# Kernel optimization log

Measured on AMD Instinct MI355X. Metric: run time of the kernel, lower is better.

Reference implementation:

```python
import jax, jax.numpy as jnp
import numpy as np

L = 12    # AttentionalGNN layers: ['self','cross'] * 6
NH = 4    # heads (hardcoded in AttentionalGNN)
D = 256   # d_model / feature_dim
B, N, M = 2, 2048, 2048
EPS = 1e-5


def conv1x1(W, b, x):
    # Conv1d(kernel_size=1): W [O, I], b [O], x [B, I, N] -> [B, O, N]
    return jnp.einsum('oi,bin->bon', W, x) + b[None, :, None]


def mha(x, src, Wq, bq, Wk, bk, Wv, bv, Wm, bm):
    b_, d_, n_ = x.shape
    dh = d_ // NH
    split = lambda t: t.reshape(b_, dh, NH, t.shape[-1])  # view(b, dim, heads, -1)
    q = split(conv1x1(Wq, bq, x))
    k = split(conv1x1(Wk, bk, src))
    v = split(conv1x1(Wv, bv, src))
    scores = jnp.einsum('bdhn,bdhm->bhnm', q, k) / dh ** 0.5
    prob = jax.nn.softmax(scores, axis=-1)
    msg = jnp.einsum('bhnm,bdhm->bdhn', prob, v).reshape(b_, d_, n_)
    return conv1x1(Wm, bm, msg)


def prop_layer(x, src, Wq, bq, Wk, bk, Wv, bv, Wm, bm, W1, b1, g, bt, W2, b2):
    msg = mha(x, src, Wq, bq, Wk, bk, Wv, bv, Wm, bm)
    h = conv1x1(W1, b1, jnp.concatenate([x, msg], axis=1))
    # BatchNorm1d in inference mode (running_mean=0, running_var=1)
    h = g[None, :, None] * (h * np.float32(1.0 / np.sqrt(1.0 + EPS))) + bt[None, :, None]
    h = jax.nn.relu(h)
    return conv1x1(W2, b2, h)


def setup_inputs() -> dict:
    key = jax.random.key(0)
    ks = jax.random.split(key, 16)
    s = 0.05
    rn = lambda k, sh: jax.random.normal(k, sh, jnp.float32) * s
    return {
        'desc0': jax.random.normal(ks[0], (B, D, N), jnp.float32),
        'desc1': jax.random.normal(ks[1], (B, D, M), jnp.float32),
        'Wq': rn(ks[2], (L, D, D)), 'bq': rn(ks[3], (L, D)),
        'Wk': rn(ks[4], (L, D, D)), 'bk': rn(ks[5], (L, D)),
        'Wv': rn(ks[6], (L, D, D)), 'bv': rn(ks[7], (L, D)),
        'Wm': rn(ks[8], (L, D, D)), 'bm': rn(ks[9], (L, D)),
        'W1': rn(ks[10], (L, 2 * D, 2 * D)), 'b1': rn(ks[11], (L, 2 * D)),
        'gamma': jnp.ones((L, 2 * D), jnp.float32),
        'beta': jnp.zeros((L, 2 * D), jnp.float32),
        'W2': rn(ks[12], (L, D, 2 * D)),
        'b2': jnp.zeros((L, D), jnp.float32),  # nn.init.constant_(mlp[-1].bias, 0)
    }


def reference(desc0, desc1, Wq, bq, Wk, bk, Wv, bv, Wm, bm, W1, b1, gamma, beta, W2, b2):
    for i in range(L):
        cross = (i % 2 == 1)
        src0, src1 = (desc1, desc0) if cross else (desc0, desc1)
        p = (Wq[i], bq[i], Wk[i], bk[i], Wv[i], bv[i], Wm[i], bm[i],
             W1[i], b1[i], gamma[i], beta[i], W2[i], b2[i])
        d0 = prop_layer(desc0, src0, *p)
        d1 = prop_layer(desc1, src1, *p)
        desc0, desc1 = desc0 + d0, desc1 + d1
    return (desc0, desc1)
```

## Files before the change

### kernel.cpp

```cpp
#include <hip/hip_runtime.h>

typedef unsigned short bf16;
typedef __attribute__((ext_vector_type(8))) short bf16x8;
typedef __attribute__((ext_vector_type(4))) float f32x4;
typedef unsigned short u16x4 __attribute__((ext_vector_type(4)));

#define DEVFN static __device__ __forceinline__

#define NL 12

#define VMW(N) asm volatile("s_waitcnt vmcnt(" #N ")" ::: "memory")
#define RBAR() asm volatile("s_barrier" ::: "memory")
#define SCHB() __builtin_amdgcn_sched_barrier(0)

DEVFN unsigned short f2bf(float f) {
  union { float f; unsigned u; } v; v.f = f;
  unsigned u = v.u;
  unsigned r = (u + 0x7fffu + ((u >> 16) & 1u)) >> 16;
  return (unsigned short)r;
}
DEVFN float bf2f(unsigned short h) {
  union { unsigned u; float f; } v; v.u = ((unsigned)h) << 16; return v.f;
}
DEVFN void tsplit(float v, unsigned short& h, unsigned short& l) {
  union { float f; unsigned u; } a; a.f = v;
  h = (unsigned short)(a.u >> 16);
  union { float f; unsigned u; } b; b.u = a.u & 0xffff0000u;
  union { float f; unsigned u; } c; c.f = v - b.f;
  l = (unsigned short)(c.u >> 16);
}
DEVFN void gll16(const bf16* g, bf16* l) {
  __builtin_amdgcn_global_load_lds(
      (const __attribute__((address_space(1))) unsigned int*)g,
      (__attribute__((address_space(3))) unsigned int*)l, 16, 0, 0);
}

#define MFMA_BF16(a, b, c) __builtin_amdgcn_mfma_f32_16x16x32_bf16((a), (b), (c), 0, 0, 0)

__global__ void prep_weights(const float* __restrict__ Wq, const float* __restrict__ bq,
                             const float* __restrict__ Wk, const float* __restrict__ bk,
                             const float* __restrict__ Wv, const float* __restrict__ bv,
                             const float* __restrict__ Wm, const float* __restrict__ bm,
                             const float* __restrict__ W1, const float* __restrict__ b1,
                             const float* __restrict__ gm, const float* __restrict__ bt,
                             const float* __restrict__ W2, const float* __restrict__ b2,
                             bf16* __restrict__ Wbf, float* __restrict__ bias)
{
  int l = blockIdx.y;
  bf16* wl = Wbf + (size_t)l * 1310720;
  float* bl = bias + l * 2304;
  int j = blockIdx.x * blockDim.x + threadIdx.x;
  if (j >= 592128) return;
  const float INV = 1.0f / sqrtf(1.0f + 1e-5f);
  const float Cs = 0.18033688011112042f;

  float w;
  size_t oh, ol;
  if (j < 196608) {
    int t = j >> 16;
    int p = (j >> 8) & 255;
    int k = j & 255;
    int c = ((p & 63) << 2) | (p >> 6);
    const float* W = (t == 0) ? Wq : (t == 1) ? Wk : Wv;
    w = W[(size_t)l * 65536 + c * 256 + k];
    if (t == 0) w *= Cs;
    oh = j; ol = j + 196608;
  } else if (j < 458752) {
    int j2 = j - 196608;
    w = W1[(size_t)l * 262144 + j2];
    oh = 524288 + j2; ol = 786432 + j2;
  } else if (j < 589824) {
    int j3 = j - 458752;
    w = W2[(size_t)l * 131072 + j3];
    oh = 1048576 + j3; ol = 1179648 + j3;
  } else {
    int b = j - 589824;
    if (b < 768) {
      int t = b >> 8, p = b & 255;
      int c = ((p & 63) << 2) | (p >> 6);
      const float* bsrc = (t == 0) ? bq : (t == 1) ? bk : bv;
      bl[b] = bsrc[l * 256 + c] * ((t == 0) ? Cs : 1.0f);
    } else if (b < 1024) {
      bl[b] = bm[l * 256 + (b - 768)];
    } else if (b < 1536) {
      bl[b] = gm[l * 512 + (b - 1024)] * INV;
    } else if (b < 2048) {
      int o = b - 1536;
      bl[b] = gm[l * 512 + o] * INV * b1[l * 512 + o] + bt[l * 512 + o];
    } else {
      bl[b] = b2[l * 256 + (b - 2048)];
    }
    return;
  }
  unsigned short hi = f2bf(w);
  wl[oh] = hi;
  wl[ol] = f2bf(w - bf2f(hi));
}

__global__ void prep_fold(const float* __restrict__ W1, const float* __restrict__ Wm,
                          const float* __restrict__ bm,
                          bf16* __restrict__ Wbf, float* __restrict__ bias)
{
  int l = blockIdx.y;
  int r0 = blockIdx.x * 8;
  int k = threadIdx.x;
  __shared__ float w1b[8][256];
  for (int j = threadIdx.x; j < 2048; j += 256)
    w1b[j >> 8][j & 255] = W1[(size_t)l * 262144 + (r0 + (j >> 8)) * 512 + 256 + (j & 255)];
  __syncthreads();
  float acc[8] = {0.f, 0.f, 0.f, 0.f, 0.f, 0.f, 0.f, 0.f};
  const float* wmrow = Wm + (size_t)l * 65536 + k;
  for (int oc = 0; oc < 256; oc++) {
    float wv = wmrow[oc * 256];
    #pragma unroll
    for (int j = 0; j < 8; j++) acc[j] += w1b[j][oc] * wv;
  }
  int p = ((k & 3) << 6) | (k >> 2);
  bf16* wl = Wbf + (size_t)l * 1310720;
  #pragma unroll
  for (int j = 0; j < 8; j++) {
    unsigned short hi = f2bf(acc[j]);
    wl[524288 + (size_t)(r0 + j) * 512 + 256 + p] = hi;
    wl[786432 + (size_t)(r0 + j) * 512 + 256 + p] = f2bf(acc[j] - bf2f(hi));
  }
  if (threadIdx.x < 8) {
    int j = threadIdx.x;
    float d = 0.f;
    for (int oc = 0; oc < 256; oc++) d += w1b[j][oc] * bm[l * 256 + oc];
    float ge = bias[l * 2304 + 1024 + r0 + j];
    bias[l * 2304 + 1536 + r0 + j] += ge * d;
  }
}

__global__ void transpose_in(const float* __restrict__ s0, const float* __restrict__ s1,
                             float* __restrict__ Dm, bf16* __restrict__ Hin,
                             bf16* __restrict__ XMl)
{
  __shared__ float t[32][33];
  int db = blockIdx.z;
  int dsc = db >> 1, bi = db & 1;
  const float* src = dsc ? s1 : s0;
  int n0 = blockIdx.x * 32, d0 = blockIdx.y * 32;
  int tx = threadIdx.x, ty = threadIdx.y;
  #pragma unroll
  for (int i = 0; i < 32; i += 8)
    t[ty + i][tx] = src[(size_t)(bi * 256 + d0 + ty + i) * 2048 + n0 + tx];
  __syncthreads();
  #pragma unroll
  for (int i = 0; i < 32; i += 8) {
    size_t xi = (size_t)db * 2048 + n0 + ty + i;
    float v = t[tx][ty + i];
    Dm[xi * 256 + d0 + tx] = v;
    unsigned short hi, lo;
    tsplit(v, hi, lo);
    Hin[xi * 512 + d0 + tx] = hi;
    XMl[xi * 512 + d0 + tx] = lo;
  }
}

__global__ void transpose_out(const float* __restrict__ Dm, float* __restrict__ out)
{
  __shared__ float t[32][33];
  int db = blockIdx.z;
  int n0 = blockIdx.x * 32, d0 = blockIdx.y * 32;
  int tx = threadIdx.x, ty = threadIdx.y;
  #pragma unroll
  for (int i = 0; i < 32; i += 8)
    t[ty + i][tx] = Dm[((size_t)db * 2048 + n0 + ty + i) * 256 + d0 + tx];
  __syncthreads();
  #pragma unroll
  for (int i = 0; i < 32; i += 8)
    out[(size_t)(db * 256 + d0 + ty + i) * 2048 + n0 + tx] = t[tx][ty + i];
}

DEVFN int gsw2(int row, int g) { return row * 32 + (((g ^ (row >> 1)) & 3) << 3); }

template<int EPI, int NT>
__global__ __launch_bounds__(256, (NT == 128) ? 2 : 3) void gemm3(
    const bf16* __restrict__ Ah, int lda,
    const bf16* __restrict__ Al, int ldal,
    const bf16* __restrict__ Wh, const bf16* __restrict__ Wl, int K,
    const float* __restrict__ b0, const float* __restrict__ b1,
    bf16* __restrict__ o0, bf16* __restrict__ o1,
    bf16* __restrict__ o2, bf16* __restrict__ o3,
    bf16* __restrict__ o4, bf16* __restrict__ o5,
    float* __restrict__ of)
{
  constexpr int NFR = NT / 32;
  __shared__ bf16 AsH[2][4096];
  __shared__ bf16 AsL[2][4096];
  __shared__ bf16 BsH[2][NT * 32];
  __shared__ bf16 BsL[2][NT * 32];
  int tid = threadIdx.x, lane = tid & 63, wid = tid >> 6;
  int wr = wid >> 1, wc = wid & 1;
  int m0 = blockIdx.x * 128, n0 = blockIdx.y * NT;

  int lrow = lane >> 2;
  int g4 = (((lane & 3) ^ (lane >> 3)) & 3) << 3;
  const bf16* A0h = Ah + (size_t)(m0 + wid * 16 + lrow) * lda + g4;
  const bf16* A0l = Al + (size_t)(m0 + wid * 16 + lrow) * ldal + g4;
  const bf16* B0h = Wh + (size_t)(n0 + wid * 16 + lrow) * K + g4;
  const bf16* B0l = Wl + (size_t)(n0 + wid * 16 + lrow) * K + g4;
  size_t a64h = (size_t)64 * lda, a64l = (size_t)64 * ldal, b64 = (size_t)64 * K;

  auto issue = [&](int k0, int b) {
    gll16(A0h + k0, &AsH[b][wid * 512]);
    gll16(A0h + a64h + k0, &AsH[b][2048 + wid * 512]);
    gll16(A0l + k0, &AsL[b][wid * 512]);
    gll16(A0l + a64l + k0, &AsL[b][2048 + wid * 512]);
    gll16(B0h + k0, &BsH[b][wid * 512]);
    gll16(B0l + k0, &BsL[b][wid * 512]);
    if constexpr (NT == 128) {
      gll16(B0h + b64 + k0, &BsH[b][2048 + wid * 512]);
      gll16(B0l + b64 + k0, &BsL[b][2048 + wid * 512]);
    }
  };

  f32x4 zero = {0.f, 0.f, 0.f, 0.f};
  f32x4 acc[4][NFR];
  #pragma unroll
  for (int i = 0; i < 4; i++)
    #pragma unroll
    for (int j = 0; j < NFR; j++) acc[i][j] = zero;

  int fr = lane & 15, g = lane >> 4;
  int cb = wc * (NT / 2);
  int nk = K >> 5;

  issue(0, 0);
  for (int ks = 0; ks < nk; ks++) {
    int cur = ks & 1;
    if (ks + 1 < nk) {
      issue((ks + 1) << 5, cur ^ 1);
      if constexpr (NT == 128) VMW(8); else VMW(6);
    } else {
      VMW(0);
    }
    RBAR(); SCHB();
    bf16x8 afh[4], afl[4], bfh[NFR], bfl[NFR];
    #pragma unroll
    for (int i = 0; i < 4; i++) {
      afh[i] = *(const bf16x8*)(&AsH[cur][gsw2(wr * 64 + i * 16 + fr, g)]);
      afl[i] = *(const bf16x8*)(&AsL[cur][gsw2(wr * 64 + i * 16 + fr, g)]);
    }
    #pragma unroll
    for (int i = 0; i < NFR; i++) {
      bfh[i] = *(const bf16x8*)(&BsH[cur][gsw2(cb + i * 16 + fr, g)]);
      bfl[i] = *(const bf16x8*)(&BsL[cur][gsw2(cb + i * 16 + fr, g)]);
    }
    #pragma unroll
    for (int mi = 0; mi < 4; mi++)
      #pragma unroll
      for (int ni = 0; ni < NFR; ni++) {
        acc[mi][ni] = MFMA_BF16(afh[mi], bfh[ni], acc[mi][ni]);
        acc[mi][ni] = MFMA_BF16(afl[mi], bfh[ni], acc[mi][ni]);
        acc[mi][ni] = MFMA_BF16(afh[mi], bfl[ni], acc[mi][ni]);
      }
    RBAR();
  }

  #pragma unroll
  for (int mi = 0; mi < 4; mi++) {
    #pragma unroll
    for (int ni = 0; ni < NFR; ni++) {
      int mrow = m0 + wr * 64 + mi * 16 + ((lane >> 4) << 2);
      int ocol = n0 + cb + ni * 16 + fr;
      if constexpr (EPI == 0) {
        float bb = b0[ocol];
        if (ocol < 512) {
          bf16* Dh = (ocol < 256) ? o0 : o2;
          bf16* Dl = (ocol < 256) ? o1 : o3;
          int oo = ocol & 255;
          #pragma unroll
          for (int r = 0; r < 4; r++) {
            unsigned short hi, lo;
            tsplit(acc[mi][ni][r] + bb, hi, lo);
            Dh[(size_t)(mrow + r) * 256 + oo] = hi;
            Dl[(size_t)(mrow + r) * 256 + oo] = lo;
          }
        } else {
          int c = ocol - 512;
          int dbi = mrow >> 11, nn = mrow & 2047;
          u16x4 ph, pl;
          #pragma unroll
          for (int r = 0; r < 4; r++) {
            unsigned short hi, lo;
            tsplit(acc[mi][ni][r] + bb, hi, lo);
            ph[r] = hi; pl[r] = lo;
          }
          *(u16x4*)(&o4[((size_t)dbi * 256 + c) * 2048 + nn]) = ph;
          *(u16x4*)(&o5[((size_t)dbi * 256 + c) * 2048 + nn]) = pl;
        }
      } else if constexpr (EPI == 3) {
        float ge = b0[ocol], be = b1[ocol];
        #pragma unroll
        for (int r = 0; r < 4; r++) {
          unsigned short hi, lo;
          tsplit(fmaxf(ge * acc[mi][ni][r] + be, 0.f), hi, lo);
          o0[(size_t)(mrow + r) * 512 + ocol] = hi;
          o1[(size_t)(mrow + r) * 512 + ocol] = lo;
        }
      } else {
        float bb = b0[ocol];
        #pragma unroll
        for (int r = 0; r < 4; r++) {
          size_t ix = (size_t)(mrow + r) * 256 + ocol;
          float d = of[ix] + acc[mi][ni][r] + bb;
          of[ix] = d;
          unsigned short hi, lo;
          tsplit(d, hi, lo);
          o0[(size_t)(mrow + r) * 512 + ocol] = hi;
          o1[(size_t)(mrow + r) * 512 + ocol] = lo;
        }
      }
    }
  }
}

DEVFN int swz(int row, int col) { return row * 64 + (col ^ ((row & 7) << 3)); }

__global__ __launch_bounds__(512, 4) void attn3s(
    const bf16* __restrict__ Qh, const bf16* __restrict__ Ql,
    const bf16* __restrict__ Kh, const bf16* __restrict__ Kl,
    const bf16* __restrict__ Vth, const bf16* __restrict__ Vtl,
    float* __restrict__ Pacc, float* __restrict__ Ml, int cross)
{
  __shared__ bf16 Ksh[64 * 64];
  __shared__ bf16 Ksl[64 * 64];
  __shared__ bf16 Vsh[64 * 64];
  __shared__ bf16 Vsl[64 * 64];
  __shared__ bf16 Psh[8][1024];
  __shared__ bf16 Psl[8][1024];
  int tid = threadIdx.x, lane = tid & 63, w = tid >> 6;
  int inst = blockIdx.y;
  int half = blockIdx.z;
  int db = inst >> 2, hd = inst & 3;
  int dsc = db >> 1, bi = db & 1;
  int sdb = (cross ? (1 - dsc) : dsc) * 2 + bi;
  size_t xq = (size_t)db * 2048;
  size_t xs = (size_t)sdb * 2048 + half * 1024;
  int n0 = blockIdx.x * 128;

  int fr = lane & 15, g = lane >> 4, kof = g << 3;

  bf16x8 aqh[2], aql[2];
  #pragma unroll
  for (int kf = 0; kf < 2; kf++) {
    size_t gx = (xq + n0 + w * 16 + fr) * 256 + hd * 64 + kf * 32 + kof;
    aqh[kf] = *(const bf16x8*)(Qh + gx);
    aql[kf] = *(const bf16x8*)(Ql + gx);
  }

  f32x4 zero = {0.f, 0.f, 0.f, 0.f};
  f32x4 oacc[4];
  #pragma unroll
  for (int ni = 0; ni < 4; ni++) oacc[ni] = zero;
  float mrun = -3.0e38f, lrun = 0.f;

  int lrow = lane >> 3;
  int g8 = ((lane & 7) ^ (lrow & 7)) << 3;
  int krow = w * 8 + lrow;
  const bf16* Ksrc_h = Kh + (xs + krow) * 256 + hd * 64 + g8;
  const bf16* Ksrc_l = Kl + (xs + krow) * 256 + hd * 64 + g8;
  const bf16* Vsrc_h = Vth + ((size_t)sdb * 256 + hd * 64 + krow) * 2048 + half * 1024 + g8;
  const bf16* Vsrc_l = Vtl + ((size_t)sdb * 256 + hd * 64 + krow) * 2048 + half * 1024 + g8;
  bf16* LKh = Ksh + w * 512;
  bf16* LKl = Ksl + w * 512;
  bf16* LVh = Vsh + w * 512;
  bf16* LVl = Vsl + w * 512;

  gll16(Ksrc_h, LKh);
  gll16(Ksrc_l, LKl);
  gll16(Vsrc_h, LVh);
  gll16(Vsrc_l, LVl);

  for (int t = 0; t < 16; t++) {
    VMW(4);
    RBAR(); SCHB();

    f32x4 sacc[4];
    #pragma unroll
    for (int ni = 0; ni < 4; ni++) sacc[ni] = zero;
    #pragma unroll
    for (int kf = 0; kf < 2; kf++) {
      #pragma unroll
      for (int ni = 0; ni < 4; ni++) {
        bf16x8 bkh = *(const bf16x8*)(&Ksh[swz(ni * 16 + fr, kf * 32 + kof)]);
        bf16x8 bkl = *(const bf16x8*)(&Ksl[swz(ni * 16 + fr, kf * 32 + kof)]);
        sacc[ni] = MFMA_BF16(bkh, aqh[kf], sacc[ni]);
        sacc[ni] = MFMA_BF16(bkh, aql[kf], sacc[ni]);
        sacc[ni] = MFMA_BF16(bkl, aqh[kf], sacc[ni]);
      }
    }

    float tml = fmaxf(fmaxf(fmaxf(sacc[0][0], sacc[0][1]), fmaxf(sacc[0][2], sacc[0][3])),
               fmaxf(fmaxf(fmaxf(sacc[1][0], sacc[1][1]), fmaxf(sacc[1][2], sacc[1][3])),
               fmaxf(fmaxf(fmaxf(sacc[2][0], sacc[2][1]), fmaxf(sacc[2][2], sacc[2][3])),
                     fmaxf(fmaxf(sacc[3][0], sacc[3][1]), fmaxf(sacc[3][2], sacc[3][3])))));
    bool need = (tml > mrun + 8.0f);
    if (__ballot(need)) {
      float tm = fmaxf(tml, __shfl_xor(tml, 16));
      tm = fmaxf(tm, __shfl_xor(tm, 32));
      float mn = fmaxf(mrun, tm);
      float s = exp2f(mrun - mn);
      mrun = mn;
      lrun *= s;
      #pragma unroll
      for (int r = 0; r < 4; r++) {
        float sr = __shfl(s, (g << 2) + r);
        #pragma unroll
        for (int ni = 0; ni < 4; ni++) oacc[ni][r] *= sr;
      }
    }
    float sum = 0.f;
    #pragma unroll
    for (int ni = 0; ni < 4; ni++)
      #pragma unroll
      for (int r = 0; r < 4; r++) {
        float pv = exp2f(sacc[ni][r] - mrun);
        sacc[ni][r] = pv;
        sum += pv;
      }
    sum += __shfl_xor(sum, 16);
    sum += __shfl_xor(sum, 32);
    lrun += sum;

    VMW(0);
    RBAR(); SCHB();

    if (t + 1 < 16) {
      gll16(Ksrc_h + (size_t)(t + 1) * 16384, LKh);
      gll16(Ksrc_l + (size_t)(t + 1) * 16384, LKl);
    }

    bf16* Pwh = &Psh[w][0];
    bf16* Pwl = &Psl[w][0];
    #pragma unroll
    for (int ni = 0; ni < 4; ni++) {
      #pragma unroll
      for (int rr = 0; rr < 2; rr++) {
        unsigned short h0, l0, h1, l1;
        tsplit(sacc[ni][2 * rr], h0, l0);
        tsplit(sacc[ni][2 * rr + 1], h1, l1);
        int key = ni * 16 + (g << 2) + 2 * rr;
        int off = swz(fr, key);
        *(unsigned*)(&Pwh[off]) = (unsigned)h0 | ((unsigned)h1 << 16);
        *(unsigned*)(&Pwl[off]) = (unsigned)l0 | ((unsigned)l1 << 16);
      }
    }

    #pragma unroll
    for (int kf = 0; kf < 2; kf++) {
      bf16x8 pah = *(const bf16x8*)(&Pwh[swz(fr, kf * 32 + kof)]);
      bf16x8 pal = *(const bf16x8*)(&Pwl[swz(fr, kf * 32 + kof)]);
      #pragma unroll
      for (int ni = 0; ni < 4; ni++) {
        bf16x8 bvh = *(const bf16x8*)(&Vsh[swz(ni * 16 + fr, kf * 32 + kof)]);
        bf16x8 bvl = *(const bf16x8*)(&Vsl[swz(ni * 16 + fr, kf * 32 + kof)]);
        oacc[ni] = MFMA_BF16(pah, bvh, oacc[ni]);
        oacc[ni] = MFMA_BF16(pal, bvh, oacc[ni]);
        oacc[ni] = MFMA_BF16(pah, bvl, oacc[ni]);
      }
    }

    RBAR();
    if (t + 1 < 16) {
      gll16(Vsrc_h + (t + 1) * 64, LVh);
      gll16(Vsrc_l + (t + 1) * 64, LVl);
    }
  }

  float* Pb = Pacc + (size_t)half * 8192 * 256;
  #pragma unroll
  for (int r = 0; r < 4; r++) {
    int nrow = n0 + w * 16 + (g << 2) + r;
    size_t row = xq + nrow;
    #pragma unroll
    for (int ni = 0; ni < 4; ni++)
      Pb[row * 256 + hd * 64 + ni * 16 + fr] = oacc[ni][r];
  }
  if (lane < 16) {
    size_t row = xq + n0 + w * 16 + lane;
    float* mp = Ml + ((row * 4 + hd) << 2) + half * 2;
    mp[0] = mrun;
    mp[1] = lrun;
  }
}

__global__ __launch_bounds__(256) void attn_combine(
    const float* __restrict__ Pacc, const float* __restrict__ Ml,
    bf16* __restrict__ Hin, bf16* __restrict__ XMl)
{
  int tid = threadIdx.x, lane = tid & 63, w = tid >> 6;
  size_t row = (size_t)blockIdx.x * 4 + w;
  int hd = lane >> 4;
  int c0 = lane * 4;
  const float* mp = Ml + ((row * 4 + hd) << 2);
  float ma = mp[0], la = mp[1], mb = mp[2], lb = mp[3];
  float m = fmaxf(ma, mb);
  float wa = exp2f(ma - m), wb = exp2f(mb - m);
  float inv = 1.0f / (la * wa + lb * wb);
  wa *= inv; wb *= inv;
  f32x4 pa = *(const f32x4*)(Pacc + row * 256 + c0);
  f32x4 pb = *(const f32x4*)(Pacc + (size_t)8192 * 256 + row * 256 + c0);
  u16x4 vh, vl;
  #pragma unroll
  for (int r = 0; r < 4; r++) {
    unsigned short hi, lo;
    tsplit(pa[r] * wa + pb[r] * wb, hi, lo);
    vh[r] = hi; vl[r] = lo;
  }
  *(u16x4*)(Hin + row * 512 + 256 + c0) = vh;
  *(u16x4*)(XMl + row * 512 + 256 + c0) = vl;
}

extern "C" void kernel_launch(void* const* d_in, const int* in_sizes, int n_in,
                              void* d_out, int out_size, void* d_ws, size_t ws_size,
                              hipStream_t stream)
{
  (void)in_sizes; (void)n_in; (void)out_size; (void)ws_size;
  const float* desc0 = (const float*)d_in[0];
  const float* desc1 = (const float*)d_in[1];
  const float* Wq = (const float*)d_in[2];
  const float* bq = (const float*)d_in[3];
  const float* Wk = (const float*)d_in[4];
  const float* bk = (const float*)d_in[5];
  const float* Wv = (const float*)d_in[6];
  const float* bv = (const float*)d_in[7];
  const float* Wm = (const float*)d_in[8];
  const float* bm = (const float*)d_in[9];
  const float* W1 = (const float*)d_in[10];
  const float* b1 = (const float*)d_in[11];
  const float* gm = (const float*)d_in[12];
  const float* bt = (const float*)d_in[13];
  const float* W2 = (const float*)d_in[14];
  const float* b2 = (const float*)d_in[15];
  float* out = (float*)d_out;

  char* ws = (char*)d_ws;
  bf16*  Wbf  = (bf16*)(ws + 0);
  float* bias = (float*)(ws + 31457280);
  float* Dm   = (float*)(ws + 31567872);
  bf16*  Hin  = (bf16*)(ws + 48345088);
  bf16*  XMl  = (bf16*)(ws + 65122304);
  bf16*  Qh   = (bf16*)(ws + 81899520);
  bf16*  Ql   = (bf16*)(ws + 90288128);
  bf16*  Kh   = (bf16*)(ws + 98676736);
  bf16*  Kl   = (bf16*)(ws + 107065344);
  bf16*  Vth  = (bf16*)(ws + 115453952);
  bf16*  Vtl  = (bf16*)(ws + 123842560);
  float* Pacc = (float*)(ws + 132231168);
  float* Ml   = (float*)(ws + 149008384);
  bf16*  Hbh  = Qh;
  bf16*  Hbl  = Kh;

  prep_weights<<<dim3(2313, 12), 256, 0, stream>>>(Wq, bq, Wk, bk, Wv, bv, Wm, bm,
                                                   W1, b1, gm, bt, W2, b2, Wbf, bias);
  prep_fold<<<dim3(64, 12), 256, 0, stream>>>(W1, Wm, bm, Wbf, bias);
  transpose_in<<<dim3(64, 8, 4), dim3(32, 8), 0, stream>>>(desc0, desc1, Dm, Hin, XMl);

  for (int l = 0; l < NL; l++) {
    const bf16* wl = Wbf + (size_t)l * 1310720;
    const float* bl = bias + l * 2304;
    int cross = l & 1;
    gemm3<0, 128><<<dim3(64, 6), 256, 0, stream>>>(Hin, 512, XMl, 512,
        wl, wl + 196608, 256, bl, nullptr,
        Qh, Ql, Kh, Kl, Vth, Vtl, nullptr);
    attn3s<<<dim3(16, 16, 2), 512, 0, stream>>>(Qh, Ql, Kh, Kl, Vth, Vtl,
                                                Pacc, Ml, cross);
    attn_combine<<<2048, 256, 0, stream>>>(Pacc, Ml, Hin, XMl);
    gemm3<3, 128><<<dim3(64, 4), 256, 0, stream>>>(Hin, 512, XMl, 512,
        wl + 524288, wl + 786432, 512, bl + 1024, bl + 1536,
        Hbh, Hbl, nullptr, nullptr, nullptr, nullptr, nullptr);
    gemm3<4, 64><<<dim3(64, 4), 256, 0, stream>>>(Hbh, 512, Hbl, 512,
        wl + 1048576, wl + 1179648, 512, bl + 2048, nullptr,
        Hin, XMl, nullptr, nullptr, nullptr, nullptr, Dm);
  }
  transpose_out<<<dim3(64, 8, 4), dim3(32, 8), 0, stream>>>(Dm, out);
}
```

Before: 1.578 ms.

## Drop split-KV attention and fuse softmax normalization into attention epilogue

The attention kernel no longer splits the key dimension into two halves. Each block now walks all 32 key tiles and normalizes its output directly, writing the bf16 hi/lo message into Hin/XMl, so the separate combine kernel and its fp32 partial buffers are gone. This removes one launch per layer and the global round trip through the partials. In exchange the grid shrinks from 512 to 256 blocks, which lowers parallelism on a large GPU. The P tile stores are also packed into 4-element vector writes.

```diff
diff --git a/kernel.cpp b/kernel.cpp
--- a/kernel.cpp
+++ b/kernel.cpp
@@ -323,7 +323,7 @@
     const bf16* __restrict__ Qh, const bf16* __restrict__ Ql,
     const bf16* __restrict__ Kh, const bf16* __restrict__ Kl,
     const bf16* __restrict__ Vth, const bf16* __restrict__ Vtl,
-    float* __restrict__ Pacc, float* __restrict__ Ml, int cross)
+    bf16* __restrict__ Hin, bf16* __restrict__ XMl, int cross)
 {
   __shared__ bf16 Ksh[64 * 64];
   __shared__ bf16 Ksl[64 * 64];
@@ -333,12 +333,11 @@
   __shared__ bf16 Psl[8][1024];
   int tid = threadIdx.x, lane = tid & 63, w = tid >> 6;
   int inst = blockIdx.y;
-  int half = blockIdx.z;
   int db = inst >> 2, hd = inst & 3;
   int dsc = db >> 1, bi = db & 1;
   int sdb = (cross ? (1 - dsc) : dsc) * 2 + bi;
   size_t xq = (size_t)db * 2048;
-  size_t xs = (size_t)sdb * 2048 + half * 1024;
+  size_t xs = (size_t)sdb * 2048;
   int n0 = blockIdx.x * 128;
 
   int fr = lane & 15, g = lane >> 4, kof = g << 3;
@@ -362,8 +361,8 @@
   int krow = w * 8 + lrow;
   const bf16* Ksrc_h = Kh + (xs + krow) * 256 + hd * 64 + g8;
   const bf16* Ksrc_l = Kl + (xs + krow) * 256 + hd * 64 + g8;
-  const bf16* Vsrc_h = Vth + ((size_t)sdb * 256 + hd * 64 + krow) * 2048 + half * 1024 + g8;
-  const bf16* Vsrc_l = Vtl + ((size_t)sdb * 256 + hd * 64 + krow) * 2048 + half * 1024 + g8;
+  const bf16* Vsrc_h = Vth + ((size_t)sdb * 256 + hd * 64 + krow) * 2048 + g8;
+  const bf16* Vsrc_l = Vtl + ((size_t)sdb * 256 + hd * 64 + krow) * 2048 + g8;
   bf16* LKh = Ksh + w * 512;
   bf16* LKl = Ksl + w * 512;
   bf16* LVh = Vsh + w * 512;
@@ -374,7 +373,7 @@
   gll16(Vsrc_h, LVh);
   gll16(Vsrc_l, LVl);
 
-  for (int t = 0; t < 16; t++) {
+  for (int t = 0; t < 32; t++) {
     VMW(4);
     RBAR(); SCHB();
 
@@ -428,7 +427,7 @@
     VMW(0);
     RBAR(); SCHB();
 
-    if (t + 1 < 16) {
+    if (t + 1 < 32) {
       gll16(Ksrc_h + (size_t)(t + 1) * 16384, LKh);
       gll16(Ksrc_l + (size_t)(t + 1) * 16384, LKl);
     }
@@ -437,16 +436,16 @@
     bf16* Pwl = &Psl[w][0];
     #pragma unroll
     for (int ni = 0; ni < 4; ni++) {
+      u16x4 ph, pl;
       #pragma unroll
-      for (int rr = 0; rr < 2; rr++) {
-        unsigned short h0, l0, h1, l1;
-        tsplit(sacc[ni][2 * rr], h0, l0);
-        tsplit(sacc[ni][2 * rr + 1], h1, l1);
-        int key = ni * 16 + (g << 2) + 2 * rr;
-        int off = swz(fr, key);
-        *(unsigned*)(&Pwh[off]) = (unsigned)h0 | ((unsigned)h1 << 16);
-        *(unsigned*)(&Pwl[off]) = (unsigned)l0 | ((unsigned)l1 << 16);
-      }
+      for (int r = 0; r < 4; r++) {
+        unsigned short h0, l0;
+        tsplit(sacc[ni][r], h0, l0);
+        ph[r] = h0; pl[r] = l0;
+      }
+      int off = swz(fr, ni * 16 + (g << 2));
+      *(u16x4*)(&Pwh[off]) = ph;
+      *(u16x4*)(&Pwl[off]) = pl;
     }
 
     #pragma unroll
@@ -464,54 +463,26 @@
     }
 
     RBAR();
-    if (t + 1 < 16) {
+    if (t + 1 < 32) {
       gll16(Vsrc_h + (t + 1) * 64, LVh);
       gll16(Vsrc_l + (t + 1) * 64, LVl);
     }
   }
 
-  float* Pb = Pacc + (size_t)half * 8192 * 256;
+  float inv = 1.0f / lrun;
   #pragma unroll
   for (int r = 0; r < 4; r++) {
-    int nrow = n0 + w * 16 + (g << 2) + r;
-    size_t row = xq + nrow;
-    #pragma unroll
-    for (int ni = 0; ni < 4; ni++)
-      Pb[row * 256 + hd * 64 + ni * 16 + fr] = oacc[ni][r];
-  }
-  if (lane < 16) {
-    size_t row = xq + n0 + w * 16 + lane;
-    float* mp = Ml + ((row * 4 + hd) << 2) + half * 2;
-    mp[0] = mrun;
-    mp[1] = lrun;
-  }
-}
-
-__global__ __launch_bounds__(256) void attn_combine(
-    const float* __restrict__ Pacc, const float* __restrict__ Ml,
-    bf16* __restrict__ Hin, bf16* __restrict__ XMl)
-{
-  int tid = threadIdx.x, lane = tid & 63, w = tid >> 6;
-  size_t row = (size_t)blockIdx.x * 4 + w;
-  int hd = lane >> 4;
-  int c0 = lane * 4;
-  const float* mp = Ml + ((row * 4 + hd) << 2);
-  float ma = mp[0], la = mp[1], mb = mp[2], lb = mp[3];
-  float m = fmaxf(ma, mb);
-  float wa = exp2f(ma - m), wb = exp2f(mb - m);
-  float inv = 1.0f / (la * wa + lb * wb);
-  wa *= inv; wb *= inv;
-  f32x4 pa = *(const f32x4*)(Pacc + row * 256 + c0);
-  f32x4 pb = *(const f32x4*)(Pacc + (size_t)8192 * 256 + row * 256 + c0);
-  u16x4 vh, vl;
-  #pragma unroll
-  for (int r = 0; r < 4; r++) {
-    unsigned short hi, lo;
-    tsplit(pa[r] * wa + pb[r] * wb, hi, lo);
-    vh[r] = hi; vl[r] = lo;
-  }
-  *(u16x4*)(Hin + row * 512 + 256 + c0) = vh;
-  *(u16x4*)(XMl + row * 512 + 256 + c0) = vl;
+    float rinv = __shfl(inv, (g << 2) + r);
+    size_t row = xq + n0 + w * 16 + (g << 2) + r;
+    #pragma unroll
+    for (int ni = 0; ni < 4; ni++) {
+      unsigned short hi, lo;
+      tsplit(oacc[ni][r] * rinv, hi, lo);
+      size_t gx = row * 512 + 256 + hd * 64 + ni * 16 + fr;
+      Hin[gx] = hi;
+      XMl[gx] = lo;
+    }
+  }
 }
 
 extern "C" void kernel_launch(void* const* d_in, const int* in_sizes, int n_in,
@@ -549,8 +520,6 @@
   bf16*  Kl   = (bf16*)(ws + 107065344);
   bf16*  Vth  = (bf16*)(ws + 115453952);
   bf16*  Vtl  = (bf16*)(ws + 123842560);
-  float* Pacc = (float*)(ws + 132231168);
-  float* Ml   = (float*)(ws + 149008384);
   bf16*  Hbh  = Qh;
   bf16*  Hbl  = Kh;
 
@@ -566,9 +535,8 @@
     gemm3<0, 128><<<dim3(64, 6), 256, 0, stream>>>(Hin, 512, XMl, 512,
         wl, wl + 196608, 256, bl, nullptr,
         Qh, Ql, Kh, Kl, Vth, Vtl, nullptr);
-    attn3s<<<dim3(16, 16, 2), 512, 0, stream>>>(Qh, Ql, Kh, Kl, Vth, Vtl,
-                                                Pacc, Ml, cross);
-    attn_combine<<<2048, 256, 0, stream>>>(Pacc, Ml, Hin, XMl);
+    attn3s<<<dim3(16, 16), 512, 0, stream>>>(Qh, Ql, Kh, Kl, Vth, Vtl,
+                                             Hin, XMl, cross);
     gemm3<3, 128><<<dim3(64, 4), 256, 0, stream>>>(Hin, 512, XMl, 512,
         wl + 524288, wl + 786432, 512, bl + 1024, bl + 1536,
         Hbh, Hbl, nullptr, nullptr, nullptr, nullptr, nullptr);
```

Result: slower. 1.731 ms (+9.7%).
